# Performance work log

Hardware: AMD Instinct MI355X
Metric: run time of the kernel (lower is better)

The kernel has to match this reference:

```python
import jax, jax.numpy as jnp
import numpy as np

B, NQ, NK, D, H = 2, 2048, 4096, 1024, 16
HD = D // H
SCALE = HD ** -0.5
NEG = -1e20


def setup_inputs() -> dict:
    key = jax.random.key(0)
    ks = jax.random.split(key, 9)
    w_std = D ** -0.5
    return {
        "q": jax.random.normal(ks[0], (B, NQ, D), dtype=jnp.float32),
        "k": jax.random.normal(ks[1], (B, NK, D), dtype=jnp.float32),
        "v": jax.random.normal(ks[2], (B, NK, D), dtype=jnp.float32),
        "key_padding_mask": jax.random.bernoulli(ks[3], 0.1, (B, NK)),
        "Wq": jax.random.normal(ks[4], (D, D), dtype=jnp.float32) * w_std,
        "Wk": jax.random.normal(ks[5], (D, D), dtype=jnp.float32) * w_std,
        "Wv": jax.random.normal(ks[6], (D, D), dtype=jnp.float32) * w_std,
        "Wp": jax.random.normal(ks[7], (D, D), dtype=jnp.float32) * w_std,
        "bp": jax.random.normal(ks[8], (D,), dtype=jnp.float32) * 0.01,
    }


def reference(q, k, v, key_padding_mask, Wq, Wk, Wv, Wp, bp):
    # linear projections (no bias, qkv_bias=False)
    qh = (q @ Wq.T).reshape(B, NQ, H, HD).transpose(0, 2, 1, 3)  # [B,H,NQ,HD]
    kh = (k @ Wk.T).reshape(B, NK, H, HD).transpose(0, 2, 1, 3)  # [B,H,NK,HD]
    vh = (v @ Wv.T).reshape(B, NK, H, HD).transpose(0, 2, 1, 3)  # [B,H,NK,HD]
    scores = jnp.einsum("bhqd,bhkd->bhqk", qh, kh)               # [B,H,NQ,NK]
    # mask BEFORE scaling (faithful to original order), then scale + softmax
    scores = jnp.where(key_padding_mask[:, None, None, :], NEG, scores)
    attn = jax.nn.softmax(scores * SCALE, axis=-1)
    out = jnp.einsum("bhqk,bhkd->bhqd", attn, vh)                # [B,H,NQ,HD]
    out = out.transpose(0, 2, 1, 3).reshape(B, NQ, D)
    x = out @ Wp.T + bp
    return x
```

## Files before the change

### kernel.cpp

```cpp
#include <hip/hip_runtime.h>


typedef __attribute__((ext_vector_type(8))) short bf16x8;
typedef __attribute__((ext_vector_type(4))) short bf16x4;
typedef __attribute__((ext_vector_type(4))) float f32x4;
typedef __attribute__((ext_vector_type(4))) unsigned short u16x4;
typedef unsigned short u16;
typedef unsigned char u8;

#define DEV __device__ __forceinline__

DEV u16 f2bf(float f) {
  union { float f; unsigned int u; } x; x.f = f;
  unsigned int u = x.u;
  return (u16)((u + 0x7fffu + ((u >> 16) & 1u)) >> 16);
}

DEV unsigned cvt_pk_bf16(float lo, float hi) {
  unsigned r;
  asm("v_cvt_pk_bf16_f32 %0, %1, %2" : "=v"(r) : "v"(lo), "v"(hi));
  return r;
}

DEV u16x4 cvt4_bf16(float4 v) {
  union { unsigned u[2]; u16x4 s; } uu;
  uu.u[0] = cvt_pk_bf16(v.x, v.y);
  uu.u[1] = cvt_pk_bf16(v.z, v.w);
  return uu.s;
}

DEV void gload16(const void* g, void* l) {
  __builtin_amdgcn_global_load_lds(
      (const __attribute__((address_space(1))) void*)g,
      (__attribute__((address_space(3))) void*)l, 16, 0, 0);
}

#define MASK_BIAS (-1.8033688e19f)
#define FREE_BIAS (-16.0f)
#define SCALE_LOG2E 0.18033688f

__global__ void decode_mask_k(const u8* __restrict__ raw, float* __restrict__ biasf, int n) {
  int t = threadIdx.x;
  int f_off = 0, f_gt1 = 0, f_80 = 0;
  for (int i = t; i < n; i += 256) {
    u8 bv = raw[i];
    if (bv > 1) f_gt1 = 1;
    if ((i & 3) && bv) f_off = 1;
    if (((i & 3) == 0) && bv == 0x80) f_80 = 1;
  }
  int g_gt1 = __syncthreads_or(f_gt1);
  int g_off = __syncthreads_or(f_off);
  int g_80  = __syncthreads_or(f_80);
  for (int i = t; i < n; i += 256) {
    int v;
    if (g_gt1) {
      if (g_80) v = (((const u16*)raw)[i] != 0) ? 1 : 0;
      else      v = (((const float*)raw)[i] != 0.0f) ? 1 : 0;
    } else if (g_off) {
      v = raw[i] ? 1 : 0;
    } else {
      v = (((const int*)raw)[i] != 0) ? 1 : 0;
    }
    biasf[i] = v ? MASK_BIAS : FREE_BIAS;
  }
}

__global__ void cvt_all_k(
    const float* __restrict__ Wq, const float* __restrict__ Wk,
    const float* __restrict__ Wv, const float* __restrict__ Wp,
    const float* __restrict__ q, const float* __restrict__ k, const float* __restrict__ v,
    u16* __restrict__ wqb, u16* __restrict__ wkb, u16* __restrict__ wvb, u16* __restrict__ wpb,
    u16* __restrict__ qb, u16* __restrict__ kb, u16* __restrict__ vb, int total)
{
  int stride = gridDim.x * blockDim.x;
  for (int idx = blockIdx.x * blockDim.x + threadIdx.x; idx < total; idx += stride) {
    const float* src; u16* dst; int off;
    if (idx < 131072)       { src = Wq; dst = wqb; off = idx; }
    else if (idx < 262144)  { src = Wk; dst = wkb; off = idx - 131072; }
    else if (idx < 393216)  { src = Wv; dst = wvb; off = idx - 262144; }
    else if (idx < 524288)  { src = Wp; dst = wpb; off = idx - 393216; }
    else if (idx < 1048576) { src = q;  dst = qb;  off = idx - 524288; }
    else if (idx < 2097152) { src = k;  dst = kb;  off = idx - 1048576; }
    else                    { src = v;  dst = vb;  off = idx - 2097152; }
    float4 a = *reinterpret_cast<const float4*>(src + (size_t)off * 8);
    float4 b = *reinterpret_cast<const float4*>(src + (size_t)off * 8 + 4);
    union { unsigned u[4]; uint4 q4; } o;
    o.u[0] = cvt_pk_bf16(a.x, a.y); o.u[1] = cvt_pk_bf16(a.z, a.w);
    o.u[2] = cvt_pk_bf16(b.x, b.y); o.u[3] = cvt_pk_bf16(b.z, b.w);
    *reinterpret_cast<uint4*>(dst + (size_t)off * 8) = o.q4;
  }
}

template <bool ABF>
__global__ __launch_bounds__(256) void proj_fused(
    const float* __restrict__ qf32, const float* __restrict__ kf32, const float* __restrict__ vf32,
    const u16* __restrict__ qb, const u16* __restrict__ kb, const u16* __restrict__ vb,
    const u16* __restrict__ wqb, const u16* __restrict__ wkb, const u16* __restrict__ wvb,
    u16* __restrict__ qh, u16* __restrict__ kh, u16* __restrict__ vh)
{
  constexpr int K = 1024;
  __shared__ __align__(16) u16 As[128 * 32];
  __shared__ __align__(16) u16 Bs[128 * 32];
  const int tid = threadIdx.x;
  const int lane = tid & 63;
  const int w = tid >> 6;
  const int wm = w >> 1, wn = w & 1;
  const int l15 = lane & 15, lg = lane >> 4;

  int bid = blockIdx.x;
  bid = (bid & 7) * 160 + (bid >> 3);
  int seg, local;
  if (bid < 256)      { seg = 0; local = bid; }
  else if (bid < 768) { seg = 1; local = bid - 256; }
  else                { seg = 2; local = bid - 768; }
  const int bm = local >> 3, bn = local & 7;
  const float* Af = seg == 0 ? qf32 : (seg == 1 ? kf32 : vf32);
  const u16* Ab   = seg == 0 ? qb   : (seg == 1 ? kb   : vb);
  const u16* Wb   = seg == 0 ? wqb  : (seg == 1 ? wkb  : wvb);
  u16* outh       = seg == 0 ? qh   : (seg == 1 ? kh   : vh);
  const int sl = (seg == 0) ? 11 : 12;

  f32x4 acc[4][4] = {};

  for (int k0 = 0; k0 < K; k0 += 32) {
    __syncthreads();
    if constexpr (ABF) {
#pragma unroll
      for (int i = 0; i < 2; ++i) {
        int f = tid + 256 * i;
        int row = f >> 2, c = f & 3;
        gload16(Ab + (size_t)(bm * 128 + row) * K + k0 + c * 8, (char*)As + f * 16);
        gload16(Wb + (size_t)(bn * 128 + row) * K + k0 + c * 8, (char*)Bs + f * 16);
      }
    } else {
#pragma unroll
      for (int i = 0; i < 2; ++i) {
        int f = tid + 256 * i;
        int row = f >> 2, c = f & 3;
        gload16(Wb + (size_t)(bn * 128 + row) * K + k0 + c * 8, (char*)Bs + f * 16);
      }
#pragma unroll
      for (int i = 0; i < 4; ++i) {
        int f = tid + 256 * i;
        int row = f >> 3, c4 = f & 7;
        float4 va = *reinterpret_cast<const float4*>(Af + (size_t)(bm * 128 + row) * K + k0 + c4 * 4);
        *reinterpret_cast<u16x4*>((char*)As + row * 64 + c4 * 8) = cvt4_bf16(va);
      }
    }
    __syncthreads();

    bf16x8 af[4], bfr[4];
#pragma unroll
    for (int mi = 0; mi < 4; ++mi)
      af[mi] = *reinterpret_cast<const bf16x8*>((const char*)As + (wm * 64 + mi * 16 + l15) * 64 + lg * 16);
#pragma unroll
    for (int ni = 0; ni < 4; ++ni)
      bfr[ni] = *reinterpret_cast<const bf16x8*>((const char*)Bs + (wn * 64 + ni * 16 + l15) * 64 + lg * 16);
#pragma unroll
    for (int mi = 0; mi < 4; ++mi)
#pragma unroll
      for (int ni = 0; ni < 4; ++ni)
        acc[mi][ni] = __builtin_amdgcn_mfma_f32_16x16x32_bf16(af[mi], bfr[ni], acc[mi][ni], 0, 0, 0);
  }

  const int seqmask = (1 << sl) - 1;
#pragma unroll
  for (int mi = 0; mi < 4; ++mi)
#pragma unroll
    for (int ni = 0; ni < 4; ++ni)
#pragma unroll
      for (int r = 0; r < 4; ++r) {
        int m = bm * 128 + wm * 64 + mi * 16 + lg * 4 + r;
        int n = bn * 128 + wn * 64 + ni * 16 + l15;
        int b = m >> sl, ml = m & seqmask;
        int h = n >> 6, hd = n & 63;
        outh[((((size_t)b * 16 + h) << sl) + ml) * 64 + hd] = f2bf(acc[mi][ni][r]);
      }
}

__global__ __launch_bounds__(256) void attn_k(
    const u16* __restrict__ qh, const u16* __restrict__ kh, const u16* __restrict__ vh,
    const float* __restrict__ biasf, u16* __restrict__ ao)
{
  __shared__ __align__(16) u16 lds[17920];

  const int tid = threadIdx.x;
  const int lane = tid & 63;
  const int w = tid >> 6;
  const int l15 = lane & 15, lg = lane >> 4;

  int bid = blockIdx.x;
  bid = (bid & 7) * 64 + (bid >> 3);
  const int qt = bid & 15;
  const int bh = bid >> 4;
  const int b = bh >> 4, h = bh & 15;

  const size_t base_kv = (size_t)bh * 4096 * 64;

  bf16x8 qf0[2], qf1[2];
  {
    const u16* qp0 = qh + ((size_t)bh * 2048 + (size_t)qt * 128 + w * 16 + l15) * 64 + lg * 8;
    qf0[0] = *reinterpret_cast<const bf16x8*>(qp0);
    qf0[1] = *reinterpret_cast<const bf16x8*>(qp0 + 32);
    const u16* qp1 = qp0 + 64 * 64;
    qf1[0] = *reinterpret_cast<const bf16x8*>(qp1);
    qf1[1] = *reinterpret_cast<const bf16x8*>(qp1 + 32);
  }

  f32x4 o0[4] = {}, o1[4] = {};
  float lac0 = 0.f, lac1 = 0.f;

  const int kp = tid >> 3, c8v = tid & 7;
  const u16* kg = kh + base_kv + (size_t)tid * 8;
  const u16* vg = vh + base_kv + (size_t)(2 * kp) * 64 + c8v * 8;
  const float* bpt = biasf + b * 4096 + lg * 4;

  const int kcol = (tid & 7) * 8;
  const int krow0 = tid >> 3, krow1 = krow0 + 32;
  int vst[8];
#pragma unroll
  for (int j = 0; j < 8; ++j) {
    int d = c8v * 8 + j;
    vst[j] = (d * 136 + kp * 4) ^ (((d >> 3) & 7) << 3);
  }
  int vrd[4][4];
#pragma unroll
  for (int dt = 0; dt < 4; ++dt)
#pragma unroll
    for (int n = 0; n < 4; ++n) {
      int d = dt * 16 + l15;
      vrd[dt][n] = ((d * 136 + (n * 16 + lg * 4) * 2)) ^ (((d >> 3) & 7) << 3);
    }

  uint4 kr0 = *reinterpret_cast<const uint4*>(kg);
  uint4 kr1 = *reinterpret_cast<const uint4*>(kg + 2048);
  uint4 vr0 = *reinterpret_cast<const uint4*>(vg);
  uint4 vr1 = *reinterpret_cast<const uint4*>(vg + 64);
  {
    u16 (*K0)[72] = reinterpret_cast<u16(*)[72]>(lds);
    u16* V0 = lds + 4608;
    *reinterpret_cast<uint4*>(&K0[krow0][kcol]) = kr0;
    *reinterpret_cast<uint4*>(&K0[krow1][kcol]) = kr1;
    const u16* pa = reinterpret_cast<const u16*>(&vr0);
    const u16* pb = reinterpret_cast<const u16*>(&vr1);
#pragma unroll
    for (int j = 0; j < 8; ++j) {
      ushort2 t2; t2.x = pa[j]; t2.y = pb[j];
      *reinterpret_cast<ushort2*>(reinterpret_cast<char*>(V0) + vst[j]) = t2;
    }
  }
  kg += 4096; vg += 4096;
  kr0 = *reinterpret_cast<const uint4*>(kg);
  kr1 = *reinterpret_cast<const uint4*>(kg + 2048);
  vr0 = *reinterpret_cast<const uint4*>(vg);
  vr1 = *reinterpret_cast<const uint4*>(vg + 64);
  __syncthreads();

  for (int t = 0; t < 64; ++t) {
    u16* bufc = lds + (t & 1) * 8960;
    u16* bufn = lds + ((t & 1) ^ 1) * 8960;
    u16 (*Ks)[72] = reinterpret_cast<u16(*)[72]>(bufc);
    u16* Vt = bufc + 4608;

    if (t < 63) {
      u16 (*Kn)[72] = reinterpret_cast<u16(*)[72]>(bufn);
      u16* Vn = bufn + 4608;
      *reinterpret_cast<uint4*>(&Kn[krow0][kcol]) = kr0;
      *reinterpret_cast<uint4*>(&Kn[krow1][kcol]) = kr1;
      const u16* pa = reinterpret_cast<const u16*>(&vr0);
      const u16* pb = reinterpret_cast<const u16*>(&vr1);
#pragma unroll
      for (int j = 0; j < 8; ++j) {
        ushort2 t2; t2.x = pa[j]; t2.y = pb[j];
        *reinterpret_cast<ushort2*>(reinterpret_cast<char*>(Vn) + vst[j]) = t2;
      }
      if (t < 62) {
        kg += 4096; vg += 4096;
        kr0 = *reinterpret_cast<const uint4*>(kg);
        kr1 = *reinterpret_cast<const uint4*>(kg + 2048);
        vr0 = *reinterpret_cast<const uint4*>(vg);
        vr1 = *reinterpret_cast<const uint4*>(vg + 64);
      }
    }

    float4 bA[4];
#pragma unroll
    for (int n = 0; n < 4; ++n)
      bA[n] = *reinterpret_cast<const float4*>(bpt + n * 16);

    f32x4 s0[4], s1[4];
    __builtin_amdgcn_s_setprio(1);
#pragma unroll
    for (int n = 0; n < 4; ++n) {
      bf16x8 k0f = *reinterpret_cast<const bf16x8*>(&Ks[n * 16 + l15][lg * 8]);
      bf16x8 k1f = *reinterpret_cast<const bf16x8*>(&Ks[n * 16 + l15][32 + lg * 8]);
      f32x4 z0 = {};
      z0 = __builtin_amdgcn_mfma_f32_16x16x32_bf16(k0f, qf0[0], z0, 0, 0, 0);
      z0 = __builtin_amdgcn_mfma_f32_16x16x32_bf16(k1f, qf0[1], z0, 0, 0, 0);
      s0[n] = z0;
      f32x4 z1 = {};
      z1 = __builtin_amdgcn_mfma_f32_16x16x32_bf16(k0f, qf1[0], z1, 0, 0, 0);
      z1 = __builtin_amdgcn_mfma_f32_16x16x32_bf16(k1f, qf1[1], z1, 0, 0, 0);
      s1[n] = z1;
    }
    __builtin_amdgcn_s_setprio(0);

    bf16x4 pbf0[4], pbf1[4];
#pragma unroll
    for (int n = 0; n < 4; ++n) {
      float p0 = __builtin_amdgcn_exp2f(fmaf(s0[n][0], SCALE_LOG2E, bA[n].x));
      float p1 = __builtin_amdgcn_exp2f(fmaf(s0[n][1], SCALE_LOG2E, bA[n].y));
      float p2 = __builtin_amdgcn_exp2f(fmaf(s0[n][2], SCALE_LOG2E, bA[n].z));
      float p3 = __builtin_amdgcn_exp2f(fmaf(s0[n][3], SCALE_LOG2E, bA[n].w));
      lac0 += (p0 + p1) + (p2 + p3);
      union { unsigned u[2]; bf16x4 v; } uu;
      uu.u[0] = cvt_pk_bf16(p0, p1);
      uu.u[1] = cvt_pk_bf16(p2, p3);
      pbf0[n] = uu.v;
    }
#pragma unroll
    for (int n = 0; n < 4; ++n) {
      float p0 = __builtin_amdgcn_exp2f(fmaf(s1[n][0], SCALE_LOG2E, bA[n].x));
      float p1 = __builtin_amdgcn_exp2f(fmaf(s1[n][1], SCALE_LOG2E, bA[n].y));
      float p2 = __builtin_amdgcn_exp2f(fmaf(s1[n][2], SCALE_LOG2E, bA[n].z));
      float p3 = __builtin_amdgcn_exp2f(fmaf(s1[n][3], SCALE_LOG2E, bA[n].w));
      lac1 += (p0 + p1) + (p2 + p3);
      union { unsigned u[2]; bf16x4 v; } uu;
      uu.u[0] = cvt_pk_bf16(p0, p1);
      uu.u[1] = cvt_pk_bf16(p2, p3);
      pbf1[n] = uu.v;
    }

    __builtin_amdgcn_s_setprio(1);
#pragma unroll
    for (int dt = 0; dt < 4; ++dt)
#pragma unroll
      for (int n = 0; n < 4; ++n) {
        bf16x4 va = *reinterpret_cast<const bf16x4*>(
            reinterpret_cast<char*>(Vt) + vrd[dt][n]);
        o0[dt] = __builtin_amdgcn_mfma_f32_16x16x16bf16_1k(va, pbf0[n], o0[dt], 0, 0, 0);
        o1[dt] = __builtin_amdgcn_mfma_f32_16x16x16bf16_1k(va, pbf1[n], o1[dt], 0, 0, 0);
      }
    __builtin_amdgcn_s_setprio(0);

    bpt += 64;
    __syncthreads();
  }

  float lr0 = lac0;
  lr0 += __shfl_xor(lr0, 16, 64);
  lr0 += __shfl_xor(lr0, 32, 64);
  float lr1 = lac1;
  lr1 += __shfl_xor(lr1, 16, 64);
  lr1 += __shfl_xor(lr1, 32, 64);
  float rl0 = __builtin_amdgcn_rcpf(fmaxf(lr0, 1e-30f));
  float rl1 = __builtin_amdgcn_rcpf(fmaxf(lr1, 1e-30f));

  u16 (*Es)[64] = reinterpret_cast<u16(*)[64]>(lds);
#pragma unroll
  for (int dt = 0; dt < 4; ++dt) {
    unsigned a0 = cvt_pk_bf16(o0[dt][0] * rl0, o0[dt][1] * rl0);
    unsigned a1 = cvt_pk_bf16(o0[dt][2] * rl0, o0[dt][3] * rl0);
    *reinterpret_cast<unsigned*>(&Es[w * 16 + l15][dt * 16 + lg * 4]) = a0;
    *reinterpret_cast<unsigned*>(&Es[w * 16 + l15][dt * 16 + lg * 4 + 2]) = a1;
    unsigned b0 = cvt_pk_bf16(o1[dt][0] * rl1, o1[dt][1] * rl1);
    unsigned b1 = cvt_pk_bf16(o1[dt][2] * rl1, o1[dt][3] * rl1);
    *reinterpret_cast<unsigned*>(&Es[64 + w * 16 + l15][dt * 16 + lg * 4]) = b0;
    *reinterpret_cast<unsigned*>(&Es[64 + w * 16 + l15][dt * 16 + lg * 4 + 2]) = b1;
  }
  asm volatile("s_waitcnt lgkmcnt(0)" ::: "memory");
#pragma unroll
  for (int g = 0; g < 2; ++g) {
    int qr = lane >> 2, dc = (lane & 3) * 16;
    int lr = g * 64 + w * 16 + qr;
    uint4 x0 = *reinterpret_cast<const uint4*>(&Es[lr][dc]);
    uint4 x1 = *reinterpret_cast<const uint4*>(&Es[lr][dc + 8]);
    u16* dst = ao + ((size_t)b * 2048 + (size_t)qt * 128 + lr) * 1024 + h * 64 + dc;
    *reinterpret_cast<uint4*>(dst) = x0;
    *reinterpret_cast<uint4*>(dst + 8) = x1;
  }
}

__global__ __launch_bounds__(256) void out_gemm(
    const u16* __restrict__ Abf, const u16* __restrict__ Wb,
    const float* __restrict__ bias, float* __restrict__ out)
{
  constexpr int K = 1024, N = 1024;
  __shared__ __align__(16) u16 As[128 * 32];
  __shared__ __align__(16) u16 Bs[128 * 32];
  const int tid = threadIdx.x;
  const int lane = tid & 63;
  const int w = tid >> 6;
  const int wm = w >> 1, wn = w & 1;
  const int bm = blockIdx.x, bn = blockIdx.y;
  const int l15 = lane & 15, lg = lane >> 4;

  f32x4 acc[4][4] = {};

  for (int k0 = 0; k0 < K; k0 += 32) {
    __syncthreads();
#pragma unroll
    for (int i = 0; i < 2; ++i) {
      int f = tid + 256 * i;
      int row = f >> 2, c = f & 3;
      gload16(Abf + (size_t)(bm * 128 + row) * K + k0 + c * 8, (char*)As + f * 16);
      gload16(Wb + (size_t)(bn * 128 + row) * K + k0 + c * 8, (char*)Bs + f * 16);
    }
    __syncthreads();

    bf16x8 af[4], bfr[4];
#pragma unroll
    for (int mi = 0; mi < 4; ++mi)
      af[mi] = *reinterpret_cast<const bf16x8*>((const char*)As + (wm * 64 + mi * 16 + l15) * 64 + lg * 16);
#pragma unroll
    for (int ni = 0; ni < 4; ++ni)
      bfr[ni] = *reinterpret_cast<const bf16x8*>((const char*)Bs + (wn * 64 + ni * 16 + l15) * 64 + lg * 16);
#pragma unroll
    for (int mi = 0; mi < 4; ++mi)
#pragma unroll
      for (int ni = 0; ni < 4; ++ni)
        acc[mi][ni] = __builtin_amdgcn_mfma_f32_16x16x32_bf16(af[mi], bfr[ni], acc[mi][ni], 0, 0, 0);
  }

#pragma unroll
  for (int mi = 0; mi < 4; ++mi)
#pragma unroll
    for (int ni = 0; ni < 4; ++ni)
#pragma unroll
      for (int r = 0; r < 4; ++r) {
        int m = bm * 128 + wm * 64 + mi * 16 + lg * 4 + r;
        int n = bn * 128 + wn * 64 + ni * 16 + l15;
        out[(size_t)m * N + n] = acc[mi][ni][r] + bias[n];
      }
}

extern "C" void kernel_launch(void* const* d_in, const int* in_sizes, int n_in,
                              void* d_out, int out_size, void* d_ws, size_t ws_size,
                              hipStream_t stream) {
  const float* q  = (const float*)d_in[0];
  const float* k  = (const float*)d_in[1];
  const float* v  = (const float*)d_in[2];
  const u8* mask_raw = (const u8*)d_in[3];
  const float* Wq = (const float*)d_in[4];
  const float* Wk = (const float*)d_in[5];
  const float* Wv = (const float*)d_in[6];
  const float* Wp = (const float*)d_in[7];
  const float* bp = (const float*)d_in[8];
  float* out = (float*)d_out;

  char* ws = (char*)d_ws;
  u16* qh = (u16*)(ws);
  u16* kh = (u16*)(ws + 8388608);
  u16* vh = (u16*)(ws + 25165824);
  u16* ao = (u16*)(ws + 41943040);
  float* biasf = (float*)(ws + 50331648);
  u16* wqb = (u16*)(ws + 50364416);
  u16* wkb = (u16*)(ws + 52461568);
  u16* wvb = (u16*)(ws + 54558720);
  u16* wpb = (u16*)(ws + 56655872);
  u16* qb  = (u16*)(ws + 58753024);
  u16* kb  = (u16*)(ws + 67141632);
  u16* vb  = (u16*)(ws + 83918848);
  const size_t need_full = 100696064;

  const bool full = ws_size >= need_full;
  cvt_all_k<<<2048, 256, 0, stream>>>(Wq, Wk, Wv, Wp, q, k, v,
                                      wqb, wkb, wvb, wpb, qb, kb, vb,
                                      full ? 3145728 : 524288);
  decode_mask_k<<<1, 256, 0, stream>>>(mask_raw, biasf, 8192);
  if (full) {
    proj_fused<true><<<1280, 256, 0, stream>>>(q, k, v, qb, kb, vb,
                                               wqb, wkb, wvb, qh, kh, vh);
  } else {
    proj_fused<false><<<1280, 256, 0, stream>>>(q, k, v, qb, kb, vb,
                                                wqb, wkb, wvb, qh, kh, vh);
  }
  attn_k<<<512, 256, 0, stream>>>(qh, kh, vh, biasf, ao);
  out_gemm<<<dim3(32, 8), 256, 0, stream>>>(ao, wpb, bp, out);
}
```

Baseline: 225.7 us.

## Store V projection transposed and stream K/V tiles with direct-to-LDS loads

The QKV projection kernel now writes V in a head-dim-major (transposed) layout by swapping the MFMA operand order for the V segment. The attention kernel then loads K and transposed V tiles straight into XOR-swizzled LDS with async global-to-LDS loads. This removes the register staging and scalar ushort2 transpose scatter the old code used every iteration. The trade-off is scattered 2-byte stores in the projection epilogue for V and a new swizzle scheme that must stay conflict-free.

Result: slower. 280.1 us (+24.1%).

```diff
diff --git a/kernel.cpp b/kernel.cpp
--- a/kernel.cpp
+++ b/kernel.cpp
@@ -117,8 +117,6 @@
   const float* Af = seg == 0 ? qf32 : (seg == 1 ? kf32 : vf32);
   const u16* Ab   = seg == 0 ? qb   : (seg == 1 ? kb   : vb);
   const u16* Wb   = seg == 0 ? wqb  : (seg == 1 ? wkb  : wvb);
-  u16* outh       = seg == 0 ? qh   : (seg == 1 ? kh   : vh);
-  const int sl = (seg == 0) ? 11 : 12;
 
   f32x4 acc[4][4] = {};
 
@@ -156,33 +154,58 @@
 #pragma unroll
     for (int ni = 0; ni < 4; ++ni)
       bfr[ni] = *reinterpret_cast<const bf16x8*>((const char*)Bs + (wn * 64 + ni * 16 + l15) * 64 + lg * 16);
+    if (seg == 2) {
+#pragma unroll
+      for (int ni = 0; ni < 4; ++ni)
+#pragma unroll
+        for (int mi = 0; mi < 4; ++mi)
+          acc[ni][mi] = __builtin_amdgcn_mfma_f32_16x16x32_bf16(bfr[ni], af[mi], acc[ni][mi], 0, 0, 0);
+    } else {
+#pragma unroll
+      for (int mi = 0; mi < 4; ++mi)
+#pragma unroll
+        for (int ni = 0; ni < 4; ++ni)
+          acc[mi][ni] = __builtin_amdgcn_mfma_f32_16x16x32_bf16(af[mi], bfr[ni], acc[mi][ni], 0, 0, 0);
+    }
+  }
+
+  if (seg == 2) {
+#pragma unroll
+    for (int ni = 0; ni < 4; ++ni)
+#pragma unroll
+      for (int mi = 0; mi < 4; ++mi)
+#pragma unroll
+        for (int r = 0; r < 4; ++r) {
+          int nn = bn * 128 + wn * 64 + ni * 16 + lg * 4 + r;
+          int mm = bm * 128 + wm * 64 + mi * 16 + l15;
+          int h = nn >> 6, d = nn & 63;
+          int bb = mm >> 12, key = mm & 4095;
+          vh[(((size_t)(bb * 16 + h)) * 64 + d) * 4096 + key] = f2bf(acc[ni][mi][r]);
+        }
+  } else {
+    const int sl = (seg == 0) ? 11 : 12;
+    u16* outh = (seg == 0) ? qh : kh;
+    const int seqmask = (1 << sl) - 1;
 #pragma unroll
     for (int mi = 0; mi < 4; ++mi)
 #pragma unroll
       for (int ni = 0; ni < 4; ++ni)
-        acc[mi][ni] = __builtin_amdgcn_mfma_f32_16x16x32_bf16(af[mi], bfr[ni], acc[mi][ni], 0, 0, 0);
-  }
-
-  const int seqmask = (1 << sl) - 1;
-#pragma unroll
-  for (int mi = 0; mi < 4; ++mi)
-#pragma unroll
-    for (int ni = 0; ni < 4; ++ni)
-#pragma unroll
-      for (int r = 0; r < 4; ++r) {
-        int m = bm * 128 + wm * 64 + mi * 16 + lg * 4 + r;
-        int n = bn * 128 + wn * 64 + ni * 16 + l15;
-        int b = m >> sl, ml = m & seqmask;
-        int h = n >> 6, hd = n & 63;
-        outh[((((size_t)b * 16 + h) << sl) + ml) * 64 + hd] = f2bf(acc[mi][ni][r]);
-      }
+#pragma unroll
+        for (int r = 0; r < 4; ++r) {
+          int m = bm * 128 + wm * 64 + mi * 16 + lg * 4 + r;
+          int n = bn * 128 + wn * 64 + ni * 16 + l15;
+          int b = m >> sl, ml = m & seqmask;
+          int h = n >> 6, hd = n & 63;
+          outh[((((size_t)b * 16 + h) << sl) + ml) * 64 + hd] = f2bf(acc[mi][ni][r]);
+        }
+  }
 }
 
 __global__ __launch_bounds__(256) void attn_k(
     const u16* __restrict__ qh, const u16* __restrict__ kh, const u16* __restrict__ vh,
     const float* __restrict__ biasf, u16* __restrict__ ao)
 {
-  __shared__ __align__(16) u16 lds[17920];
+  __shared__ __align__(16) u16 lds[16384];
 
   const int tid = threadIdx.x;
   const int lane = tid & 63;
@@ -195,7 +218,8 @@
   const int bh = bid >> 4;
   const int b = bh >> 4, h = bh & 15;
 
-  const size_t base_kv = (size_t)bh * 4096 * 64;
+  const u16* kbase = kh + (size_t)bh * 4096 * 64;
+  const u16* vtbase = vh + (size_t)bh * 64 * 4096;
 
   bf16x8 qf0[2], qf1[2];
   {
@@ -209,78 +233,55 @@
 
   f32x4 o0[4] = {}, o1[4] = {};
   float lac0 = 0.f, lac1 = 0.f;
-
-  const int kp = tid >> 3, c8v = tid & 7;
-  const u16* kg = kh + base_kv + (size_t)tid * 8;
-  const u16* vg = vh + base_kv + (size_t)(2 * kp) * 64 + c8v * 8;
   const float* bpt = biasf + b * 4096 + lg * 4;
 
-  const int kcol = (tid & 7) * 8;
-  const int krow0 = tid >> 3, krow1 = krow0 + 32;
-  int vst[8];
-#pragma unroll
-  for (int j = 0; j < 8; ++j) {
-    int d = c8v * 8 + j;
-    vst[j] = (d * 136 + kp * 4) ^ (((d >> 3) & 7) << 3);
-  }
+  int ksrc[2], vsrc[2];
+#pragma unroll
+  for (int i = 0; i < 2; ++i) {
+    int f = tid + 256 * i;
+    int row = f >> 3, g = f & 7;
+    int gs = (g ^ (row & 7)) * 8;
+    ksrc[i] = row * 64 + gs;
+    vsrc[i] = row * 4096 + gs;
+  }
+
+  int krd[4][2];
+#pragma unroll
+  for (int n = 0; n < 4; ++n)
+#pragma unroll
+    for (int kk = 0; kk < 2; ++kk) {
+      int row = n * 16 + l15;
+      krd[n][kk] = row * 128 + (((kk * 4 + lg) ^ (row & 7)) << 4);
+    }
   int vrd[4][4];
 #pragma unroll
   for (int dt = 0; dt < 4; ++dt)
 #pragma unroll
     for (int n = 0; n < 4; ++n) {
       int d = dt * 16 + l15;
-      vrd[dt][n] = ((d * 136 + (n * 16 + lg * 4) * 2)) ^ (((d >> 3) & 7) << 3);
-    }
-
-  uint4 kr0 = *reinterpret_cast<const uint4*>(kg);
-  uint4 kr1 = *reinterpret_cast<const uint4*>(kg + 2048);
-  uint4 vr0 = *reinterpret_cast<const uint4*>(vg);
-  uint4 vr1 = *reinterpret_cast<const uint4*>(vg + 64);
+      vrd[dt][n] = d * 128 + (((2 * n + (lg >> 1)) ^ (d & 7)) << 4) + (lg & 1) * 8;
+    }
+
   {
-    u16 (*K0)[72] = reinterpret_cast<u16(*)[72]>(lds);
-    u16* V0 = lds + 4608;
-    *reinterpret_cast<uint4*>(&K0[krow0][kcol]) = kr0;
-    *reinterpret_cast<uint4*>(&K0[krow1][kcol]) = kr1;
-    const u16* pa = reinterpret_cast<const u16*>(&vr0);
-    const u16* pb = reinterpret_cast<const u16*>(&vr1);
-#pragma unroll
-    for (int j = 0; j < 8; ++j) {
-      ushort2 t2; t2.x = pa[j]; t2.y = pb[j];
-      *reinterpret_cast<ushort2*>(reinterpret_cast<char*>(V0) + vst[j]) = t2;
-    }
-  }
-  kg += 4096; vg += 4096;
-  kr0 = *reinterpret_cast<const uint4*>(kg);
-  kr1 = *reinterpret_cast<const uint4*>(kg + 2048);
-  vr0 = *reinterpret_cast<const uint4*>(vg);
-  vr1 = *reinterpret_cast<const uint4*>(vg + 64);
+    char* kb = (char*)lds;
+    char* vb0 = kb + 8192;
+    gload16(kbase + ksrc[0], kb + tid * 16);
+    gload16(kbase + ksrc[1], kb + (tid + 256) * 16);
+    gload16(vtbase + vsrc[0], vb0 + tid * 16);
+    gload16(vtbase + vsrc[1], vb0 + (tid + 256) * 16);
+  }
   __syncthreads();
 
   for (int t = 0; t < 64; ++t) {
-    u16* bufc = lds + (t & 1) * 8960;
-    u16* bufn = lds + ((t & 1) ^ 1) * 8960;
-    u16 (*Ks)[72] = reinterpret_cast<u16(*)[72]>(bufc);
-    u16* Vt = bufc + 4608;
-
+    char* basec = (char*)lds + (t & 1) * 16384;
     if (t < 63) {
-      u16 (*Kn)[72] = reinterpret_cast<u16(*)[72]>(bufn);
-      u16* Vn = bufn + 4608;
-      *reinterpret_cast<uint4*>(&Kn[krow0][kcol]) = kr0;
-      *reinterpret_cast<uint4*>(&Kn[krow1][kcol]) = kr1;
-      const u16* pa = reinterpret_cast<const u16*>(&vr0);
-      const u16* pb = reinterpret_cast<const u16*>(&vr1);
-#pragma unroll
-      for (int j = 0; j < 8; ++j) {
-        ushort2 t2; t2.x = pa[j]; t2.y = pb[j];
-        *reinterpret_cast<ushort2*>(reinterpret_cast<char*>(Vn) + vst[j]) = t2;
-      }
-      if (t < 62) {
-        kg += 4096; vg += 4096;
-        kr0 = *reinterpret_cast<const uint4*>(kg);
-        kr1 = *reinterpret_cast<const uint4*>(kg + 2048);
-        vr0 = *reinterpret_cast<const uint4*>(vg);
-        vr1 = *reinterpret_cast<const uint4*>(vg + 64);
-      }
+      char* basen = (char*)lds + ((t & 1) ^ 1) * 16384;
+      const u16* kt = kbase + (t + 1) * 4096;
+      const u16* vt = vtbase + (t + 1) * 64;
+      gload16(kt + ksrc[0], basen + tid * 16);
+      gload16(kt + ksrc[1], basen + (tid + 256) * 16);
+      gload16(vt + vsrc[0], basen + 8192 + tid * 16);
+      gload16(vt + vsrc[1], basen + 8192 + (tid + 256) * 16);
     }
 
     float4 bA[4];
@@ -292,8 +293,8 @@
     __builtin_amdgcn_s_setprio(1);
 #pragma unroll
     for (int n = 0; n < 4; ++n) {
-      bf16x8 k0f = *reinterpret_cast<const bf16x8*>(&Ks[n * 16 + l15][lg * 8]);
-      bf16x8 k1f = *reinterpret_cast<const bf16x8*>(&Ks[n * 16 + l15][32 + lg * 8]);
+      bf16x8 k0f = *reinterpret_cast<const bf16x8*>(basec + krd[n][0]);
+      bf16x8 k1f = *reinterpret_cast<const bf16x8*>(basec + krd[n][1]);
       f32x4 z0 = {};
       z0 = __builtin_amdgcn_mfma_f32_16x16x32_bf16(k0f, qf0[0], z0, 0, 0, 0);
       z0 = __builtin_amdgcn_mfma_f32_16x16x32_bf16(k1f, qf0[1], z0, 0, 0, 0);
@@ -331,13 +332,13 @@
       pbf1[n] = uu.v;
     }
 
+    char* vbc = basec + 8192;
     __builtin_amdgcn_s_setprio(1);
 #pragma unroll
     for (int dt = 0; dt < 4; ++dt)
 #pragma unroll
       for (int n = 0; n < 4; ++n) {
-        bf16x4 va = *reinterpret_cast<const bf16x4*>(
-            reinterpret_cast<char*>(Vt) + vrd[dt][n]);
+        bf16x4 va = *reinterpret_cast<const bf16x4*>(vbc + vrd[dt][n]);
         o0[dt] = __builtin_amdgcn_mfma_f32_16x16x16bf16_1k(va, pbf0[n], o0[dt], 0, 0, 0);
         o1[dt] = __builtin_amdgcn_mfma_f32_16x16x16bf16_1k(va, pbf1[n], o1[dt], 0, 0, 0);
       }
```

## Share K/V tiles across 8 waves in attention and fold mask decode into prep

Applied to the files above, without the earlier changes.

The attention kernel now runs 512-thread blocks covering 256 query rows instead of 256-thread blocks covering 128. Only the first four waves stage K/V into LDS, and all eight waves consume each staged tile. This halves global K/V reads and LDS staging per query, at the cost of fewer, larger blocks (256 in total) and more LDS pressure for the output staging. Separately, the mask-decode kernel is merged into the conversion kernel as an extra last block, which removes one kernel launch.

New measurement: 210.5 us. -6.7%, faster.

```diff
diff --git a/kernel.cpp b/kernel.cpp
--- a/kernel.cpp
+++ b/kernel.cpp
@@ -39,40 +39,41 @@
 #define FREE_BIAS (-16.0f)
 #define SCALE_LOG2E 0.18033688f
 
-__global__ void decode_mask_k(const u8* __restrict__ raw, float* __restrict__ biasf, int n) {
-  int t = threadIdx.x;
-  int f_off = 0, f_gt1 = 0, f_80 = 0;
-  for (int i = t; i < n; i += 256) {
-    u8 bv = raw[i];
-    if (bv > 1) f_gt1 = 1;
-    if ((i & 3) && bv) f_off = 1;
-    if (((i & 3) == 0) && bv == 0x80) f_80 = 1;
-  }
-  int g_gt1 = __syncthreads_or(f_gt1);
-  int g_off = __syncthreads_or(f_off);
-  int g_80  = __syncthreads_or(f_80);
-  for (int i = t; i < n; i += 256) {
-    int v;
-    if (g_gt1) {
-      if (g_80) v = (((const u16*)raw)[i] != 0) ? 1 : 0;
-      else      v = (((const float*)raw)[i] != 0.0f) ? 1 : 0;
-    } else if (g_off) {
-      v = raw[i] ? 1 : 0;
-    } else {
-      v = (((const int*)raw)[i] != 0) ? 1 : 0;
-    }
-    biasf[i] = v ? MASK_BIAS : FREE_BIAS;
-  }
-}
-
-__global__ void cvt_all_k(
+__global__ void prep_k(
     const float* __restrict__ Wq, const float* __restrict__ Wk,
     const float* __restrict__ Wv, const float* __restrict__ Wp,
     const float* __restrict__ q, const float* __restrict__ k, const float* __restrict__ v,
     u16* __restrict__ wqb, u16* __restrict__ wkb, u16* __restrict__ wvb, u16* __restrict__ wpb,
-    u16* __restrict__ qb, u16* __restrict__ kb, u16* __restrict__ vb, int total)
+    u16* __restrict__ qb, u16* __restrict__ kb, u16* __restrict__ vb, int total,
+    const u8* __restrict__ raw, float* __restrict__ biasf)
 {
-  int stride = gridDim.x * blockDim.x;
+  if (blockIdx.x == gridDim.x - 1) {
+    int t = threadIdx.x;
+    int f_off = 0, f_gt1 = 0, f_80 = 0;
+    for (int i = t; i < 8192; i += 256) {
+      u8 bv = raw[i];
+      if (bv > 1) f_gt1 = 1;
+      if ((i & 3) && bv) f_off = 1;
+      if (((i & 3) == 0) && bv == 0x80) f_80 = 1;
+    }
+    int g_gt1 = __syncthreads_or(f_gt1);
+    int g_off = __syncthreads_or(f_off);
+    int g_80  = __syncthreads_or(f_80);
+    for (int i = t; i < 8192; i += 256) {
+      int vv;
+      if (g_gt1) {
+        if (g_80) vv = (((const u16*)raw)[i] != 0) ? 1 : 0;
+        else      vv = (((const float*)raw)[i] != 0.0f) ? 1 : 0;
+      } else if (g_off) {
+        vv = raw[i] ? 1 : 0;
+      } else {
+        vv = (((const int*)raw)[i] != 0) ? 1 : 0;
+      }
+      biasf[i] = vv ? MASK_BIAS : FREE_BIAS;
+    }
+    return;
+  }
+  int stride = (gridDim.x - 1) * blockDim.x;
   for (int idx = blockIdx.x * blockDim.x + threadIdx.x; idx < total; idx += stride) {
     const float* src; u16* dst; int off;
     if (idx < 131072)       { src = Wq; dst = wqb; off = idx; }
@@ -83,10 +84,10 @@
     else if (idx < 2097152) { src = k;  dst = kb;  off = idx - 1048576; }
     else                    { src = v;  dst = vb;  off = idx - 2097152; }
     float4 a = *reinterpret_cast<const float4*>(src + (size_t)off * 8);
-    float4 b = *reinterpret_cast<const float4*>(src + (size_t)off * 8 + 4);
+    float4 bq = *reinterpret_cast<const float4*>(src + (size_t)off * 8 + 4);
     union { unsigned u[4]; uint4 q4; } o;
     o.u[0] = cvt_pk_bf16(a.x, a.y); o.u[1] = cvt_pk_bf16(a.z, a.w);
-    o.u[2] = cvt_pk_bf16(b.x, b.y); o.u[3] = cvt_pk_bf16(b.z, b.w);
+    o.u[2] = cvt_pk_bf16(bq.x, bq.y); o.u[3] = cvt_pk_bf16(bq.z, bq.w);
     *reinterpret_cast<uint4*>(dst + (size_t)off * 8) = o.q4;
   }
 }
@@ -178,7 +179,7 @@
       }
 }
 
-__global__ __launch_bounds__(256) void attn_k(
+__global__ __launch_bounds__(512, 2) void attn_k(
     const u16* __restrict__ qh, const u16* __restrict__ kh, const u16* __restrict__ vh,
     const float* __restrict__ biasf, u16* __restrict__ ao)
 {
@@ -190,31 +191,30 @@
   const int l15 = lane & 15, lg = lane >> 4;
 
   int bid = blockIdx.x;
-  bid = (bid & 7) * 64 + (bid >> 3);
-  const int qt = bid & 15;
-  const int bh = bid >> 4;
+  bid = (bid & 7) * 32 + (bid >> 3);
+  const int qt = bid & 7;
+  const int bh = bid >> 3;
   const int b = bh >> 4, h = bh & 15;
 
   const size_t base_kv = (size_t)bh * 4096 * 64;
 
   bf16x8 qf0[2], qf1[2];
   {
-    const u16* qp0 = qh + ((size_t)bh * 2048 + (size_t)qt * 128 + w * 16 + l15) * 64 + lg * 8;
+    const u16* qp0 = qh + ((size_t)bh * 2048 + (size_t)qt * 256 + w * 16 + l15) * 64 + lg * 8;
     qf0[0] = *reinterpret_cast<const bf16x8*>(qp0);
     qf0[1] = *reinterpret_cast<const bf16x8*>(qp0 + 32);
-    const u16* qp1 = qp0 + 64 * 64;
+    const u16* qp1 = qp0 + 128 * 64;
     qf1[0] = *reinterpret_cast<const bf16x8*>(qp1);
     qf1[1] = *reinterpret_cast<const bf16x8*>(qp1 + 32);
   }
 
   f32x4 o0[4] = {}, o1[4] = {};
   float lac0 = 0.f, lac1 = 0.f;
+  const float* bpt = biasf + b * 4096 + lg * 4;
 
   const int kp = tid >> 3, c8v = tid & 7;
   const u16* kg = kh + base_kv + (size_t)tid * 8;
   const u16* vg = vh + base_kv + (size_t)(2 * kp) * 64 + c8v * 8;
-  const float* bpt = biasf + b * 4096 + lg * 4;
-
   const int kcol = (tid & 7) * 8;
   const int krow0 = tid >> 3, krow1 = krow0 + 32;
   int vst[8];
@@ -232,11 +232,12 @@
       vrd[dt][n] = ((d * 136 + (n * 16 + lg * 4) * 2)) ^ (((d >> 3) & 7) << 3);
     }
 
-  uint4 kr0 = *reinterpret_cast<const uint4*>(kg);
-  uint4 kr1 = *reinterpret_cast<const uint4*>(kg + 2048);
-  uint4 vr0 = *reinterpret_cast<const uint4*>(vg);
-  uint4 vr1 = *reinterpret_cast<const uint4*>(vg + 64);
-  {
+  uint4 kr0, kr1, vr0, vr1;
+  if (w < 4) {
+    kr0 = *reinterpret_cast<const uint4*>(kg);
+    kr1 = *reinterpret_cast<const uint4*>(kg + 2048);
+    vr0 = *reinterpret_cast<const uint4*>(vg);
+    vr1 = *reinterpret_cast<const uint4*>(vg + 64);
     u16 (*K0)[72] = reinterpret_cast<u16(*)[72]>(lds);
     u16* V0 = lds + 4608;
     *reinterpret_cast<uint4*>(&K0[krow0][kcol]) = kr0;
@@ -248,21 +249,21 @@
       ushort2 t2; t2.x = pa[j]; t2.y = pb[j];
       *reinterpret_cast<ushort2*>(reinterpret_cast<char*>(V0) + vst[j]) = t2;
     }
-  }
-  kg += 4096; vg += 4096;
-  kr0 = *reinterpret_cast<const uint4*>(kg);
-  kr1 = *reinterpret_cast<const uint4*>(kg + 2048);
-  vr0 = *reinterpret_cast<const uint4*>(vg);
-  vr1 = *reinterpret_cast<const uint4*>(vg + 64);
+    kg += 4096; vg += 4096;
+    kr0 = *reinterpret_cast<const uint4*>(kg);
+    kr1 = *reinterpret_cast<const uint4*>(kg + 2048);
+    vr0 = *reinterpret_cast<const uint4*>(vg);
+    vr1 = *reinterpret_cast<const uint4*>(vg + 64);
+  }
   __syncthreads();
 
   for (int t = 0; t < 64; ++t) {
     u16* bufc = lds + (t & 1) * 8960;
-    u16* bufn = lds + ((t & 1) ^ 1) * 8960;
     u16 (*Ks)[72] = reinterpret_cast<u16(*)[72]>(bufc);
     u16* Vt = bufc + 4608;
 
-    if (t < 63) {
+    if (w < 4 && t < 63) {
+      u16* bufn = lds + ((t & 1) ^ 1) * 8960;
       u16 (*Kn)[72] = reinterpret_cast<u16(*)[72]>(bufn);
       u16* Vn = bufn + 4608;
       *reinterpret_cast<uint4*>(&Kn[krow0][kcol]) = kr0;
@@ -365,17 +366,17 @@
     *reinterpret_cast<unsigned*>(&Es[w * 16 + l15][dt * 16 + lg * 4 + 2]) = a1;
     unsigned b0 = cvt_pk_bf16(o1[dt][0] * rl1, o1[dt][1] * rl1);
     unsigned b1 = cvt_pk_bf16(o1[dt][2] * rl1, o1[dt][3] * rl1);
-    *reinterpret_cast<unsigned*>(&Es[64 + w * 16 + l15][dt * 16 + lg * 4]) = b0;
-    *reinterpret_cast<unsigned*>(&Es[64 + w * 16 + l15][dt * 16 + lg * 4 + 2]) = b1;
+    *reinterpret_cast<unsigned*>(&Es[128 + w * 16 + l15][dt * 16 + lg * 4]) = b0;
+    *reinterpret_cast<unsigned*>(&Es[128 + w * 16 + l15][dt * 16 + lg * 4 + 2]) = b1;
   }
   asm volatile("s_waitcnt lgkmcnt(0)" ::: "memory");
 #pragma unroll
   for (int g = 0; g < 2; ++g) {
     int qr = lane >> 2, dc = (lane & 3) * 16;
-    int lr = g * 64 + w * 16 + qr;
+    int lr = g * 128 + w * 16 + qr;
     uint4 x0 = *reinterpret_cast<const uint4*>(&Es[lr][dc]);
     uint4 x1 = *reinterpret_cast<const uint4*>(&Es[lr][dc + 8]);
-    u16* dst = ao + ((size_t)b * 2048 + (size_t)qt * 128 + lr) * 1024 + h * 64 + dc;
+    u16* dst = ao + ((size_t)b * 2048 + (size_t)qt * 256 + lr) * 1024 + h * 64 + dc;
     *reinterpret_cast<uint4*>(dst) = x0;
     *reinterpret_cast<uint4*>(dst + 8) = x1;
   }
@@ -464,10 +465,9 @@
   const size_t need_full = 100696064;
 
   const bool full = ws_size >= need_full;
-  cvt_all_k<<<2048, 256, 0, stream>>>(Wq, Wk, Wv, Wp, q, k, v,
-                                      wqb, wkb, wvb, wpb, qb, kb, vb,
-                                      full ? 3145728 : 524288);
-  decode_mask_k<<<1, 256, 0, stream>>>(mask_raw, biasf, 8192);
+  prep_k<<<2049, 256, 0, stream>>>(Wq, Wk, Wv, Wp, q, k, v,
+                                   wqb, wkb, wvb, wpb, qb, kb, vb,
+                                   full ? 3145728 : 524288, mask_raw, biasf);
   if (full) {
     proj_fused<true><<<1280, 256, 0, stream>>>(q, k, v, qb, kb, vb,
                                                wqb, wkb, wvb, qh, kh, vh);
@@ -475,6 +475,6 @@
     proj_fused<false><<<1280, 256, 0, stream>>>(q, k, v, qb, kb, vb,
                                                 wqb, wkb, wvb, qh, kh, vh);
   }
-  attn_k<<<512, 256, 0, stream>>>(qh, kh, vh, biasf, ao);
+  attn_k<<<256, 512, 0, stream>>>(qh, kh, vh, biasf, ao);
   out_gemm<<<dim3(32, 8), 256, 0, stream>>>(ao, wpb, bp, out);
 }
```
